# Optimization experiments

Measured on AMD Instinct MI355X. Metric: run time of the kernel, lower is better.

Reference implementation:

```python
import jax, jax.numpy as jnp
import numpy as np

B, N, C, H = 4, 2048, 1024, 16
D = C // H

def setup_inputs() -> dict:
    key = jax.random.key(0)
    k1, k2, k3 = jax.random.split(key, 3)
    x = jax.random.normal(k1, (B, N, C), dtype=jnp.float32)
    w_qkv = jax.random.normal(k2, (C, 3 * C), dtype=jnp.float32) * (C ** -0.5)
    w_proj = jax.random.normal(k3, (C, C), dtype=jnp.float32) * (C ** -0.5)
    b_proj = jnp.zeros((C,), dtype=jnp.float32)
    return {"x": x, "w_qkv": w_qkv, "w_proj": w_proj, "b_proj": b_proj}

def reference(x, w_qkv, w_proj, b_proj):
    scale = D ** -0.5
    qkv = x @ w_qkv                                   # [B,N,3C]
    qkv = qkv.reshape(B, N, 3, H, D).transpose(2, 0, 3, 1, 4)  # [3,B,H,N,D]
    q, k, v = qkv[0], qkv[1], qkv[2]
    attn = jnp.einsum('bhnd,bhmd->bhnm', q, k) * scale  # [B,H,N,N]
    attn = jax.nn.softmax(attn, axis=-1)
    o = jnp.einsum('bhnm,bhmd->bhnd', attn, v)          # [B,H,N,D]
    o = o.transpose(0, 2, 1, 3).reshape(B, N, C)
    return o @ w_proj + b_proj
```

## Files before the change

kernel.cpp:

```cpp
#include <hip/hip_runtime.h>
#include <hip/hip_bf16.h>


#define B_ 4
#define N_ 2048
#define C_ 1024
#define H_ 16
#define D_ 64
#define MCONST 24.0f

typedef __attribute__((ext_vector_type(8))) __bf16 bf16x8;
typedef __attribute__((ext_vector_type(4))) float f32x4;
typedef __attribute__((ext_vector_type(16))) float f32x16;
typedef unsigned int u32;
typedef __attribute__((ext_vector_type(2))) u32 u32x2;
typedef __attribute__((ext_vector_type(4))) u32 u32x4;

__device__ inline unsigned short f2bf(float f) {
  __bf16 h = (__bf16)f;
  return __builtin_bit_cast(unsigned short, h);
}

__device__ __forceinline__ u32 pk2(float lo, float hi) {
  return (u32)f2bf(lo) | ((u32)f2bf(hi) << 16);
}

__device__ __forceinline__ void gld16(const void* g, void* l) {
  __builtin_amdgcn_global_load_lds(
      (const __attribute__((address_space(1))) u32*)g,
      (__attribute__((address_space(3))) u32*)l, 16, 0, 0);
}

__global__ __launch_bounds__(256) void cvt_bf16_kernel(
    const float* __restrict__ in, unsigned short* __restrict__ out) {
  int i = (blockIdx.x * 256 + threadIdx.x) * 8;
  float4 f0 = *(const float4*)&in[i];
  float4 f1 = *(const float4*)&in[i + 4];
  ushort4 h0, h1;
  h0.x = f2bf(f0.x); h0.y = f2bf(f0.y); h0.z = f2bf(f0.z); h0.w = f2bf(f0.w);
  h1.x = f2bf(f1.x); h1.y = f2bf(f1.y); h1.z = f2bf(f1.z); h1.w = f2bf(f1.w);
  *(ushort4*)&out[i] = h0;
  *(ushort4*)&out[i + 4] = h1;
}

__global__ __launch_bounds__(256) void transpose_cvt_kernel(
    const float* __restrict__ in, unsigned short* __restrict__ out,
    int K, int Nn) {
  __shared__ float tile[32][33];
  const int t = threadIdx.x;
  const int k0 = blockIdx.y * 32, n0 = blockIdx.x * 32;
  {
    int r = t >> 3, c = (t & 7) * 4;
    float4 f = *(const float4*)&in[(size_t)(k0 + r) * Nn + n0 + c];
    tile[r][c + 0] = f.x; tile[r][c + 1] = f.y;
    tile[r][c + 2] = f.z; tile[r][c + 3] = f.w;
  }
  __syncthreads();
  {
    int nr = t >> 3, kc = (t & 7) * 4;
    ushort4 h;
    h.x = f2bf(tile[kc + 0][nr]);
    h.y = f2bf(tile[kc + 1][nr]);
    h.z = f2bf(tile[kc + 2][nr]);
    h.w = f2bf(tile[kc + 3][nr]);
    *(ushort4*)&out[(size_t)(n0 + nr) * K + k0 + kc] = h;
  }
}

__global__ __launch_bounds__(256) void transpose_v_kernel(
    const unsigned short* __restrict__ vb, unsigned short* __restrict__ vtb) {
  __shared__ u32 tile[64][65];
  const int tid = threadIdx.x;
  const int n0 = blockIdx.x * 64;
  const int bh = blockIdx.y;
  const size_t base = (size_t)bh * N_ * D_;
#pragma unroll
  for (int i = 0; i < 2; i++) {
    int id = i * 256 + tid;
    int row = id >> 3, c8 = id & 7;
    uint4 v = *(const uint4*)&vb[base + (size_t)(n0 + row) * D_ + c8 * 8];
    const unsigned short* pv = (const unsigned short*)&v;
#pragma unroll
    for (int j = 0; j < 8; j++) tile[row][c8 * 8 + j] = pv[j];
  }
  __syncthreads();
#pragma unroll
  for (int i = 0; i < 2; i++) {
    int id = i * 256 + tid;
    int d = id >> 3, nc = id & 7;
    uint4 o;
    unsigned short* po = (unsigned short*)&o;
#pragma unroll
    for (int j = 0; j < 8; j++) po[j] = (unsigned short)tile[nc * 8 + j][d];
    *(uint4*)&vtb[base + (size_t)d * N_ + n0 + nc * 8] = o;
  }
}

template<int MODE>
__global__ __launch_bounds__(256) void gemm128_kernel(
    const unsigned short* __restrict__ A, const unsigned short* __restrict__ Bt,
    const float* __restrict__ bias,
    unsigned short* __restrict__ qb, unsigned short* __restrict__ kb,
    unsigned short* __restrict__ vb, float* __restrict__ outp,
    int M, int K, int Nout)
{
  __shared__ unsigned short Al[128 * 64];
  __shared__ unsigned short Bl[128 * 64];
  const int tid = threadIdx.x;
  const int w = tid >> 6, lane = tid & 63;
  const int l15 = lane & 15, lk = lane >> 4;
  const int wr = w >> 1, wc = w & 1;
  const int n0 = blockIdx.x * 128, m0 = blockIdx.y * 128;
  const int srow = tid >> 3;
  const int scol = (tid & 7) * 8;

  f32x4 acc[4][4];
#pragma unroll
  for (int m = 0; m < 4; m++)
#pragma unroll
    for (int n = 0; n < 4; n++) acc[m][n] = f32x4{0.f, 0.f, 0.f, 0.f};

  for (int kt = 0; kt < K; kt += 64) {
#pragma unroll
    for (int i = 0; i < 4; i++)
      gld16(&A[(size_t)(m0 + i * 32 + srow) * K + kt + scol],
            &Al[i * 2048 + w * 512]);
#pragma unroll
    for (int i = 0; i < 4; i++)
      gld16(&Bt[(size_t)(n0 + i * 32 + srow) * K + kt + scol],
            &Bl[i * 2048 + w * 512]);
    __syncthreads();

#pragma unroll
    for (int kk = 0; kk < 2; kk++) {
      bf16x8 af[4], bf[4];
#pragma unroll
      for (int m = 0; m < 4; m++)
        af[m] = *(const bf16x8*)&Al[(wr * 64 + m * 16 + l15) * 64 + kk * 32 + lk * 8];
#pragma unroll
      for (int n = 0; n < 4; n++)
        bf[n] = *(const bf16x8*)&Bl[(wc * 64 + n * 16 + l15) * 64 + kk * 32 + lk * 8];
#pragma unroll
      for (int m = 0; m < 4; m++)
#pragma unroll
        for (int n = 0; n < 4; n++)
          acc[m][n] = __builtin_amdgcn_mfma_f32_16x16x32_bf16(af[m], bf[n], acc[m][n], 0, 0, 0);
    }
    __syncthreads();
  }

  if (MODE == 0) {
#pragma unroll
    for (int n = 0; n < 4; n++) {
      int c = n0 + wc * 64 + n * 16 + l15;
      int tsel = c >> 10, h = (c >> 6) & 15, d = c & 63;
      unsigned short* dst = (tsel == 0) ? qb : (tsel == 1 ? kb : vb);
      float sc = (tsel == 0) ? 0.125f * 1.44269504088896340736f : 1.0f;
#pragma unroll
      for (int m = 0; m < 4; m++) {
#pragma unroll
        for (int r = 0; r < 4; r++) {
          int row = m0 + wr * 64 + m * 16 + lk * 4 + r;
          int b = row >> 11, nn = row & 2047;
          dst[(((size_t)(b * 16 + h)) * 2048 + nn) * 64 + d] = f2bf(acc[m][n][r] * sc);
        }
      }
    }
  } else {
#pragma unroll
    for (int n = 0; n < 4; n++) {
      int c = n0 + wc * 64 + n * 16 + l15;
      float bv = bias[c];
#pragma unroll
      for (int m = 0; m < 4; m++) {
#pragma unroll
        for (int r = 0; r < 4; r++) {
          int row = m0 + wr * 64 + m * 16 + lk * 4 + r;
          outp[(size_t)row * Nout + c] = acc[m][n][r] + bv;
        }
      }
    }
  }
}

__global__ __launch_bounds__(512) void flash_kernel(
    const unsigned short* __restrict__ qb, const unsigned short* __restrict__ kb,
    const unsigned short* __restrict__ vtb, unsigned short* __restrict__ ob)
{
  __shared__ unsigned short KVs[2][2][64 * 64];
  __shared__ float Lf[2][128];
  float* scratch = (float*)&KVs[0][0][0];

  const int tid = threadIdx.x;
  const int w = tid >> 6;
  const int lane = tid & 63;
  const int l31 = lane & 31;
  const int hi = lane >> 5;
  const int g = w >> 2;
  const int ws = w & 3;
  const int q0 = blockIdx.x * 128;
  const int bh = blockIdx.y;
  const size_t base = (size_t)bh * N_ * D_;
  const unsigned short* Qg = qb + base;
  const unsigned short* Kg = kb + base;
  const unsigned short* Vtg = vtb + base;

  const int t8 = tid & 255;
  const int s_r = t8 >> 3;
  const int s_sl = (t8 & 7) ^ (s_r & 7);
  const int swz = (lane & 7) << 3;
  unsigned short* Kl = &KVs[g][0][0];
  unsigned short* Vl = &KVs[g][1][0];

  const int qrow_g = q0 + ws * 32 + l31;
  bf16x8 qf[4];
#pragma unroll
  for (int ds = 0; ds < 4; ds++)
    qf[ds] = *(const bf16x8*)&Qg[(size_t)qrow_g * 64 + ds * 16 + hi * 8];

  f32x16 acc0, acc1, minit;
#pragma unroll
  for (int i = 0; i < 16; i++) { acc0[i] = 0.f; acc1[i] = 0.f; minit[i] = -MCONST; }
  float lrow = 0.f;

  const int kvbeg = g * (N_ / 2);
  for (int kv0 = kvbeg; kv0 < kvbeg + N_ / 2; kv0 += 64) {
#pragma unroll
    for (int i = 0; i < 2; i++)
      gld16(&Kg[(size_t)(kv0 + i * 32 + s_r) * 64 + s_sl * 8],
            &Kl[i * 2048 + ws * 512]);
#pragma unroll
    for (int i = 0; i < 2; i++)
      gld16(&Vtg[(size_t)(i * 32 + s_r) * N_ + kv0 + s_sl * 8],
            &Vl[i * 2048 + ws * 512]);
    __syncthreads();

    u32 F[4][4];
#pragma unroll
    for (int t = 0; t < 2; t++) {
      f32x16 sa = minit;
      __builtin_amdgcn_s_setprio(1);
#pragma unroll
      for (int ds = 0; ds < 4; ds++) {
        bf16x8 a = *(const bf16x8*)&Kl[(t * 32 + l31) * 64 + ((ds * 16 + hi * 8) ^ swz)];
        sa = __builtin_amdgcn_mfma_f32_32x32x16_bf16(a, qf[ds], sa, 0, 0, 0);
      }
      __builtin_amdgcn_s_setprio(0);

      float p[16];
#pragma unroll
      for (int r = 0; r < 16; r++) p[r] = __builtin_amdgcn_exp2f(sa[r]);
      lrow += ((p[0] + p[1]) + (p[2] + p[3])) + ((p[4] + p[5]) + (p[6] + p[7]))
            + ((p[8] + p[9]) + (p[10] + p[11])) + ((p[12] + p[13]) + (p[14] + p[15]));

      u32 pk[8];
#pragma unroll
      for (int j = 0; j < 8; j++) pk[j] = pk2(p[2 * j], p[2 * j + 1]);
#if __has_builtin(__builtin_amdgcn_permlane32_swap)
      u32x2 r02 = __builtin_amdgcn_permlane32_swap(pk[0], pk[2], false, false);
      u32x2 r13 = __builtin_amdgcn_permlane32_swap(pk[1], pk[3], false, false);
      u32x2 r46 = __builtin_amdgcn_permlane32_swap(pk[4], pk[6], false, false);
      u32x2 r57 = __builtin_amdgcn_permlane32_swap(pk[5], pk[7], false, false);
      F[2 * t][0] = r02[0]; F[2 * t][2] = r02[1];
      F[2 * t][1] = r13[0]; F[2 * t][3] = r13[1];
      F[2 * t + 1][0] = r46[0]; F[2 * t + 1][2] = r46[1];
      F[2 * t + 1][1] = r57[0]; F[2 * t + 1][3] = r57[1];
#else
      u32 sw[8];
#pragma unroll
      for (int j = 0; j < 8; j++) sw[j] = (u32)__shfl_xor((int)pk[j], 32);
      F[2 * t][0] = hi ? sw[2] : pk[0];
      F[2 * t][1] = hi ? sw[3] : pk[1];
      F[2 * t][2] = hi ? pk[2] : sw[0];
      F[2 * t][3] = hi ? pk[3] : sw[1];
      F[2 * t + 1][0] = hi ? sw[6] : pk[4];
      F[2 * t + 1][1] = hi ? sw[7] : pk[5];
      F[2 * t + 1][2] = hi ? pk[6] : sw[4];
      F[2 * t + 1][3] = hi ? pk[7] : sw[5];
#endif
    }

    __builtin_amdgcn_s_setprio(1);
#pragma unroll
    for (int ks = 0; ks < 4; ks++) {
      u32x4 fv = {F[ks][0], F[ks][1], F[ks][2], F[ks][3]};
      bf16x8 a = __builtin_bit_cast(bf16x8, fv);
      bf16x8 b0 = *(const bf16x8*)&Vl[(0 * 32 + l31) * 64 + ((ks * 16 + hi * 8) ^ swz)];
      acc0 = __builtin_amdgcn_mfma_f32_32x32x16_bf16(a, b0, acc0, 0, 0, 0);
      bf16x8 b1 = *(const bf16x8*)&Vl[(1 * 32 + l31) * 64 + ((ks * 16 + hi * 8) ^ swz)];
      acc1 = __builtin_amdgcn_mfma_f32_32x32x16_bf16(a, b1, acc1, 0, 0, 0);
    }
    __builtin_amdgcn_s_setprio(0);
    __syncthreads();
  }

  float rs = lrow + __shfl_xor(lrow, 32);
  if (lane < 32) Lf[g][ws * 32 + l31] = rs;
  __syncthreads();

  if (g == 0) {
#pragma unroll
    for (int r = 0; r < 16; r++) {
      int qr = (r & 3) + 8 * (r >> 2) + 4 * hi;
      scratch[(ws * 32 + qr) * 64 + l31]      = acc0[r];
      scratch[(ws * 32 + qr) * 64 + 32 + l31] = acc1[r];
    }
  }
  __syncthreads();
  if (g == 1) {
    const int b = bh >> 4, h = bh & 15;
#pragma unroll
    for (int r = 0; r < 16; r++) {
      int qr = (r & 3) + 8 * (r >> 2) + 4 * hi;
      float inv = 1.0f / (Lf[0][ws * 32 + qr] + Lf[1][ws * 32 + qr]);
      float o0 = scratch[(ws * 32 + qr) * 64 + l31]      + acc0[r];
      float o1 = scratch[(ws * 32 + qr) * 64 + 32 + l31] + acc1[r];
      int nq = q0 + ws * 32 + qr;
      size_t ob0 = (((size_t)b * N_ + nq) * H_ + h) * D_;
      ob[ob0 + l31]      = f2bf(o0 * inv);
      ob[ob0 + 32 + l31] = f2bf(o1 * inv);
    }
  }
}

extern "C" void kernel_launch(void* const* d_in, const int* in_sizes, int n_in,
                              void* d_out, int out_size, void* d_ws, size_t ws_size,
                              hipStream_t stream) {
  const float* x      = (const float*)d_in[0];
  const float* w_qkv  = (const float*)d_in[1];
  const float* w_proj = (const float*)d_in[2];
  const float* b_proj = (const float*)d_in[3];
  float* out = (float*)d_out;

  const size_t qsz = (size_t)B_ * H_ * N_ * D_;
  unsigned short* qb     = (unsigned short*)d_ws;
  unsigned short* kb     = qb + qsz;
  unsigned short* vb     = kb + qsz;
  unsigned short* vtb    = vb + qsz;
  unsigned short* xbf    = vtb + qsz;
  unsigned short* ob     = xbf;
  unsigned short* wqkv_t = xbf + qsz;
  unsigned short* wproj_t= wqkv_t + (size_t)3072 * 1024;

  cvt_bf16_kernel<<<4096, 256, 0, stream>>>(x, xbf);
  transpose_cvt_kernel<<<dim3(3072 / 32, 1024 / 32), 256, 0, stream>>>(w_qkv, wqkv_t, 1024, 3072);
  transpose_cvt_kernel<<<dim3(1024 / 32, 1024 / 32), 256, 0, stream>>>(w_proj, wproj_t, 1024, 1024);

  gemm128_kernel<0><<<dim3(3072 / 128, 8192 / 128), 256, 0, stream>>>(
      xbf, wqkv_t, nullptr, qb, kb, vb, nullptr, 8192, 1024, 3072);

  transpose_v_kernel<<<dim3(N_ / 64, B_ * H_), 256, 0, stream>>>(vb, vtb);

  flash_kernel<<<dim3(N_ / 128, B_ * H_), 512, 0, stream>>>(qb, kb, vtb, ob);

  gemm128_kernel<1><<<dim3(1024 / 128, 8192 / 128), 256, 0, stream>>>(
      ob, wproj_t, b_proj, nullptr, nullptr, nullptr, out, 8192, 1024, 1024);
}
```

Before: 223.2 us.

## Double-buffer K/V tiles in LDS to overlap loads with MFMA compute

```diff
diff --git a/kernel.cpp b/kernel.cpp
--- a/kernel.cpp
+++ b/kernel.cpp
@@ -187,9 +187,9 @@
     const unsigned short* __restrict__ qb, const unsigned short* __restrict__ kb,
     const unsigned short* __restrict__ vtb, unsigned short* __restrict__ ob)
 {
-  __shared__ unsigned short KVs[2][2][64 * 64];
+  __shared__ unsigned short KVs[2][2][2][64 * 64];
   __shared__ float Lf[2][128];
-  float* scratch = (float*)&KVs[0][0][0];
+  float* scratch = (float*)&KVs[0][0][0][0];
 
   const int tid = threadIdx.x;
   const int w = tid >> 6;
@@ -209,8 +209,6 @@
   const int s_r = t8 >> 3;
   const int s_sl = (t8 & 7) ^ (s_r & 7);
   const int swz = (lane & 7) << 3;
-  unsigned short* Kl = &KVs[g][0][0];
-  unsigned short* Vl = &KVs[g][1][0];
 
   const int qrow_g = q0 + ws * 32 + l31;
   bf16x8 qf[4];
@@ -224,16 +222,34 @@
   float lrow = 0.f;
 
   const int kvbeg = g * (N_ / 2);
-  for (int kv0 = kvbeg; kv0 < kvbeg + N_ / 2; kv0 += 64) {
-#pragma unroll
-    for (int i = 0; i < 2; i++)
-      gld16(&Kg[(size_t)(kv0 + i * 32 + s_r) * 64 + s_sl * 8],
-            &Kl[i * 2048 + ws * 512]);
-#pragma unroll
-    for (int i = 0; i < 2; i++)
-      gld16(&Vtg[(size_t)(i * 32 + s_r) * N_ + kv0 + s_sl * 8],
-            &Vl[i * 2048 + ws * 512]);
+
+#pragma unroll
+  for (int i = 0; i < 2; i++)
+    gld16(&Kg[(size_t)(kvbeg + i * 32 + s_r) * 64 + s_sl * 8],
+          &KVs[g][0][0][i * 2048 + ws * 512]);
+#pragma unroll
+  for (int i = 0; i < 2; i++)
+    gld16(&Vtg[(size_t)(i * 32 + s_r) * N_ + kvbeg + s_sl * 8],
+          &KVs[g][0][1][i * 2048 + ws * 512]);
+
+  int cur = 0;
+  for (int it = 0; it < 16; ++it) {
     __syncthreads();
+
+    if (it + 1 < 16) {
+      int kvn = kvbeg + (it + 1) * 64;
+#pragma unroll
+      for (int i = 0; i < 2; i++)
+        gld16(&Kg[(size_t)(kvn + i * 32 + s_r) * 64 + s_sl * 8],
+              &KVs[g][cur ^ 1][0][i * 2048 + ws * 512]);
+#pragma unroll
+      for (int i = 0; i < 2; i++)
+        gld16(&Vtg[(size_t)(i * 32 + s_r) * N_ + kvn + s_sl * 8],
+              &KVs[g][cur ^ 1][1][i * 2048 + ws * 512]);
+    }
+
+    const unsigned short* Kl = &KVs[g][cur][0][0];
+    const unsigned short* Vl = &KVs[g][cur][1][0];
 
     u32 F[4][4];
 #pragma unroll
@@ -291,7 +307,7 @@
       acc1 = __builtin_amdgcn_mfma_f32_32x32x16_bf16(a, b1, acc1, 0, 0, 0);
     }
     __builtin_amdgcn_s_setprio(0);
-    __syncthreads();
+    cur ^= 1;
   }
 
   float rs = lrow + __shfl_xor(lrow, 32);
```

Result: no change. 224.0 us (+0.4%).
